# Kernel tuning notes

Hardware: AMD Instinct MI355X
Metric: run time of the kernel (lower is better)

The kernel has to match this reference:

```python
import jax, jax.numpy as jnp
import numpy as np

N0, N1, N2, N3, N4 = 50000, 150000, 20000, 5000, 1000
E0, E1, NNZ01 = 800000, 1500000, 300000
D, CCI = 64, 3


def _xavier(key, shape):
    fan_in, fan_out = shape[0], shape[-1]
    s = jnp.sqrt(2.0 / (fan_in + fan_out)).astype(jnp.float32)
    return jax.random.normal(key, shape, dtype=jnp.float32) * s


def setup_inputs() -> dict:
    ks = jax.random.split(jax.random.key(0), 24)
    return {
        "x_0": jax.random.normal(ks[0], (N0, D), jnp.float32),
        "x_1": jax.random.normal(ks[1], (N1, D), jnp.float32),
        "x_2": jax.random.normal(ks[2], (N2, D), jnp.float32),
        "x_3": jax.random.normal(ks[3], (N3, D), jnp.float32),
        "x_4": jax.random.normal(ks[4], (N4, D), jnp.float32),
        "adjacency_0_idx": jax.random.randint(ks[5], (2, E0), 0, N0),
        "adjacency_0_val": jax.random.uniform(ks[6], (E0,), jnp.float32),
        "adjacency_1_idx": jax.random.randint(ks[7], (2, E1), 0, N1),
        "adjacency_1_val": jax.random.uniform(ks[8], (E1,), jnp.float32),
        "incidence_0_1_idx": jnp.stack([
            jax.random.randint(ks[9], (NNZ01,), 0, N0),   # row: 0-cells
            jax.random.randint(ks[10], (NNZ01,), 0, N1),  # col: 1-cells
        ]),
        "incidence_0_1_val": jax.random.uniform(ks[11], (NNZ01,), jnp.float32),
        "cci_0_to_0": jax.random.normal(ks[12], (E0, CCI), jnp.float32),
        "cci_1_to_1": jax.random.normal(ks[13], (E1, CCI), jnp.float32),
        "W_hbs0": _xavier(ks[14], (D, D)),
        "a_hbs0": _xavier(ks[15], (CCI,)),
        "W_hbs1": _xavier(ks[16], (D, D)),
        "a_hbs1": _xavier(ks[17], (CCI,)),
        "W_hbns_s": _xavier(ks[18], (D, D)),
        "W_hbns_t": _xavier(ks[19], (D, D)),
        "W_aggr0": _xavier(ks[20], (D, D)),
        "W_aggr1": _xavier(ks[21], (D, D)),
    }


def _hbs(x, idx, val, cci, W, a):
    # same-rank message passing: m = xW, per-nonzero coeff = A_val * (cci . a)
    m = x @ W                                    # (N, D)
    coeff = val * (cci @ a)                      # (E,)
    msg = coeff[:, None] * m[idx[0]]             # gather source rows (E, D)
    return jax.nn.relu(jax.ops.segment_sum(msg, idx[1], num_segments=x.shape[0]))


def reference(x_0, x_1, x_2, x_3, x_4,
              adjacency_0_idx, adjacency_0_val,
              adjacency_1_idx, adjacency_1_val,
              incidence_0_1_idx, incidence_0_1_val,
              cci_0_to_0, cci_1_to_1,
              W_hbs0, a_hbs0, W_hbs1, a_hbs1,
              W_hbns_s, W_hbns_t, W_aggr0, W_aggr1):
    # HBS blocks (rank 0 -> 0 and 1 -> 1)
    x_0_to_0 = _hbs(x_0, adjacency_0_idx, adjacency_0_val, cci_0_to_0, W_hbs0, a_hbs0)
    x_1_to_1 = _hbs(x_1, adjacency_1_idx, adjacency_1_val, cci_1_to_1, W_hbs1, a_hbs1)

    # HBNS block across incidence_0_1 (rows index 0-cells, cols index 1-cells)
    row, col = incidence_0_1_idx[0], incidence_0_1_idx[1]
    ms = x_1 @ W_hbns_s                          # source (1-cell) messages
    mt = x_0 @ W_hbns_t                          # target (0-cell) messages
    v = incidence_0_1_val[:, None]
    x_1_to_0 = jax.nn.relu(jax.ops.segment_sum(v * ms[col], row, num_segments=x_0.shape[0]))
    x_0_to_1 = jax.nn.relu(jax.ops.segment_sum(v * mt[row], col, num_segments=x_1.shape[0]))

    # RankAggregator: sum sources, linear map, update
    x_0_level1 = jax.nn.relu((x_0_to_0 + x_1_to_0) @ W_aggr0)
    x_1_level1 = jax.nn.relu((x_1_to_1 + x_0_to_1) @ W_aggr1)
    return (x_0_level1, x_1_level1, x_2, x_3, x_4)
```

## Files before the change

kernel.cpp:

```cpp
#include <hip/hip_runtime.h>

constexpr int N0 = 50000, N1 = 150000, N2 = 20000, N3 = 5000, N4 = 1000;
constexpr int E0 = 800000, E1 = 1500000, NNZ01 = 300000;
constexpr int D = 64;

__global__ __launch_bounds__(256) void gemm64(const float* __restrict__ x,
                                              const float* __restrict__ W,
                                              float* __restrict__ y, int n) {
    __shared__ float Ws[64][64];
    __shared__ float Xs[64][64];
    const int t = threadIdx.x;
    for (int i = t; i < 64 * 64; i += 256) Ws[i >> 6][i & 63] = W[i];
    const long row0 = (long)blockIdx.x * 64;
    const int nrow = min(64, n - (int)row0);
    {
        const float4* xv = (const float4*)(x + row0 * D);
        float4* xs = (float4*)&Xs[0][0];
        for (int i = t; i < nrow * 16; i += 256) xs[i] = xv[i];
    }
    __syncthreads();
    const int r0 = (t >> 4) * 4;
    const int c  = (t & 15) * 4;
    float acc[4][4] = {};
#pragma unroll
    for (int k = 0; k < 64; ++k) {
        const float4 w = *(const float4*)&Ws[k][c];
#pragma unroll
        for (int rr = 0; rr < 4; ++rr) {
            const float xv = Xs[r0 + rr][k];
            acc[rr][0] = fmaf(xv, w.x, acc[rr][0]);
            acc[rr][1] = fmaf(xv, w.y, acc[rr][1]);
            acc[rr][2] = fmaf(xv, w.z, acc[rr][2]);
            acc[rr][3] = fmaf(xv, w.w, acc[rr][3]);
        }
    }
#pragma unroll
    for (int rr = 0; rr < 4; ++rr) {
        const long row = row0 + r0 + rr;
        if (row < n) {
            *(float4*)(y + row * D + c) =
                make_float4(acc[rr][0], acc[rr][1], acc[rr][2], acc[rr][3]);
        }
    }
}

__global__ __launch_bounds__(256) void gemm64_aggr(const float* __restrict__ A,
                                                   const float* __restrict__ B,
                                                   const float* __restrict__ W,
                                                   float* __restrict__ y, int n) {
    __shared__ float Ws[64][64];
    __shared__ float Xs[64][64];
    const int t = threadIdx.x;
    for (int i = t; i < 64 * 64; i += 256) Ws[i >> 6][i & 63] = W[i];
    const long row0 = (long)blockIdx.x * 64;
    const int nrow = min(64, n - (int)row0);
    {
        const float4* av = (const float4*)(A + row0 * D);
        const float4* bv = (const float4*)(B + row0 * D);
        float4* xs = (float4*)&Xs[0][0];
        for (int i = t; i < nrow * 16; i += 256) {
            const float4 p = av[i];
            const float4 q = bv[i];
            float4 r;
            r.x = fmaxf(p.x, 0.f) + fmaxf(q.x, 0.f);
            r.y = fmaxf(p.y, 0.f) + fmaxf(q.y, 0.f);
            r.z = fmaxf(p.z, 0.f) + fmaxf(q.z, 0.f);
            r.w = fmaxf(p.w, 0.f) + fmaxf(q.w, 0.f);
            xs[i] = r;
        }
    }
    __syncthreads();
    const int r0 = (t >> 4) * 4;
    const int c  = (t & 15) * 4;
    float acc[4][4] = {};
#pragma unroll
    for (int k = 0; k < 64; ++k) {
        const float4 w = *(const float4*)&Ws[k][c];
#pragma unroll
        for (int rr = 0; rr < 4; ++rr) {
            const float xv = Xs[r0 + rr][k];
            acc[rr][0] = fmaf(xv, w.x, acc[rr][0]);
            acc[rr][1] = fmaf(xv, w.y, acc[rr][1]);
            acc[rr][2] = fmaf(xv, w.z, acc[rr][2]);
            acc[rr][3] = fmaf(xv, w.w, acc[rr][3]);
        }
    }
#pragma unroll
    for (int rr = 0; rr < 4; ++rr) {
        const long row = row0 + r0 + rr;
        if (row < n) {
            float4 o;
            o.x = fmaxf(acc[rr][0], 0.f);
            o.y = fmaxf(acc[rr][1], 0.f);
            o.z = fmaxf(acc[rr][2], 0.f);
            o.w = fmaxf(acc[rr][3], 0.f);
            *(float4*)(y + row * D + c) = o;
        }
    }
}

__global__ __launch_bounds__(256) void hbs_scatter(const int* __restrict__ src,
                                                   const int* __restrict__ dst,
                                                   const float* __restrict__ val,
                                                   const float* __restrict__ cci,
                                                   const float* __restrict__ a,
                                                   const float* __restrict__ m,
                                                   float* __restrict__ acc, int ne) {
    const int e = blockIdx.x * 4 + (threadIdx.x >> 6);
    if (e >= ne) return;
    const int lane = threadIdx.x & 63;
    const int s = src[e];
    const int d = dst[e];
    const float coeff =
        val[e] * (cci[(size_t)e * 3 + 0] * a[0] + cci[(size_t)e * 3 + 1] * a[1] +
                  cci[(size_t)e * 3 + 2] * a[2]);
    atomicAdd(&acc[(size_t)d * D + lane], coeff * m[(size_t)s * D + lane]);
}

__global__ __launch_bounds__(256) void hbns_scatter(const int* __restrict__ rowi,
                                                    const int* __restrict__ coli,
                                                    const float* __restrict__ val,
                                                    const float* __restrict__ ms,
                                                    const float* __restrict__ mt,
                                                    float* __restrict__ acc10,
                                                    float* __restrict__ acc01, int ne) {
    const int e = blockIdx.x * 4 + (threadIdx.x >> 6);
    if (e >= ne) return;
    const int lane = threadIdx.x & 63;
    const int r = rowi[e];
    const int c = coli[e];
    const float v = val[e];
    atomicAdd(&acc10[(size_t)r * D + lane], v * ms[(size_t)c * D + lane]);
    atomicAdd(&acc01[(size_t)c * D + lane], v * mt[(size_t)r * D + lane]);
}

extern "C" void kernel_launch(void* const* d_in, const int* in_sizes, int n_in,
                              void* d_out, int out_size, void* d_ws, size_t ws_size,
                              hipStream_t stream) {
    const float* x0    = (const float*)d_in[0];
    const float* x1    = (const float*)d_in[1];
    const float* x2    = (const float*)d_in[2];
    const float* x3    = (const float*)d_in[3];
    const float* x4    = (const float*)d_in[4];
    const int*   adj0  = (const int*)d_in[5];
    const float* adj0v = (const float*)d_in[6];
    const int*   adj1  = (const int*)d_in[7];
    const float* adj1v = (const float*)d_in[8];
    const int*   inc01 = (const int*)d_in[9];
    const float* incv  = (const float*)d_in[10];
    const float* cci0  = (const float*)d_in[11];
    const float* cci1  = (const float*)d_in[12];
    const float* Whbs0 = (const float*)d_in[13];
    const float* ahbs0 = (const float*)d_in[14];
    const float* Whbs1 = (const float*)d_in[15];
    const float* ahbs1 = (const float*)d_in[16];
    const float* Wns_s = (const float*)d_in[17];
    const float* Wns_t = (const float*)d_in[18];
    const float* Wagg0 = (const float*)d_in[19];
    const float* Wagg1 = (const float*)d_in[20];

    float* out = (float*)d_out;
    float* ws  = (float*)d_ws;

    const size_t S0 = (size_t)N0 * D;
    const size_t S1 = (size_t)N1 * D;

    const size_t full_bytes = (2 * S0 + 2 * S1) * 2 * sizeof(float);
    float *m0, *m1, *msb, *mtb, *acc00, *acc11, *acc10, *acc01;
    if (ws_size >= full_bytes) {
        m0 = ws;            m1 = m0 + S0;
        msb = m1 + S1;      mtb = msb + S1;
        acc00 = mtb + S0;   acc11 = acc00 + S0;
        acc10 = acc11 + S1; acc01 = acc10 + S0;
    } else {
        m0 = out;           m1 = out + S0;
        msb = ws;           mtb = msb + S1;
        acc00 = mtb + S0;   acc11 = acc00 + S0;
        acc10 = acc11 + S1; acc01 = acc10 + S0;
    }

    hipMemsetAsync(acc00, 0, (2 * S0 + 2 * S1) * sizeof(float), stream);

    gemm64<<<(N0 + 63) / 64, 256, 0, stream>>>(x0, Whbs0, m0, N0);
    gemm64<<<(N1 + 63) / 64, 256, 0, stream>>>(x1, Whbs1, m1, N1);
    gemm64<<<(N1 + 63) / 64, 256, 0, stream>>>(x1, Wns_s, msb, N1);
    gemm64<<<(N0 + 63) / 64, 256, 0, stream>>>(x0, Wns_t, mtb, N0);

    hbs_scatter<<<(E0 + 3) / 4, 256, 0, stream>>>(adj0, adj0 + E0, adj0v, cci0,
                                                  ahbs0, m0, acc00, E0);
    hbs_scatter<<<(E1 + 3) / 4, 256, 0, stream>>>(adj1, adj1 + E1, adj1v, cci1,
                                                  ahbs1, m1, acc11, E1);
    hbns_scatter<<<(NNZ01 + 3) / 4, 256, 0, stream>>>(inc01, inc01 + NNZ01, incv,
                                                      msb, mtb, acc10, acc01, NNZ01);

    gemm64_aggr<<<(N0 + 63) / 64, 256, 0, stream>>>(acc00, acc10, Wagg0, out, N0);
    gemm64_aggr<<<(N1 + 63) / 64, 256, 0, stream>>>(acc11, acc01, Wagg1, out + S0, N1);

    hipMemcpyAsync(out + S0 + S1, x2, (size_t)N2 * D * sizeof(float),
                   hipMemcpyDeviceToDevice, stream);
    hipMemcpyAsync(out + S0 + S1 + (size_t)N2 * D, x3, (size_t)N3 * D * sizeof(float),
                   hipMemcpyDeviceToDevice, stream);
    hipMemcpyAsync(out + S0 + S1 + (size_t)(N2 + N3) * D, x4,
                   (size_t)N4 * D * sizeof(float), hipMemcpyDeviceToDevice, stream);
}
```

Baseline: 1.140 ms.

## Replace atomic edge scatter with CSR counting-sort and per-node segmented gather

Builds per-destination CSR offsets on each call: an integer histogram, a three-pass prefix scan, then an atomic-cursor reorder of edge ids. The float per-lane atomic scatter is replaced by a per-node wavefront gather that accumulates in registers and fuses the ReLU. The aggregation GEMM then reads the pre-summed buffer written into the output in place, which drops the zeroing memset of large accumulators. The cost is several extra launches plus integer atomics for the sort, and the workspace-size fallback path is removed.

```diff
diff --git a/kernel.cpp b/kernel.cpp
--- a/kernel.cpp
+++ b/kernel.cpp
@@ -4,6 +4,12 @@
 constexpr int E0 = 800000, E1 = 1500000, NNZ01 = 300000;
 constexpr int D = 64;
 
+constexpr int TOT_NODES = 2 * N0 + 2 * N1;
+constexpr int OFFN = TOT_NODES + 1;
+constexpr int SCAN_CHUNK = 2048;
+constexpr int NB = (OFFN + SCAN_CHUNK - 1) / SCAN_CHUNK;
+
+template <bool RELU_STORE>
 __global__ __launch_bounds__(256) void gemm64(const float* __restrict__ x,
                                               const float* __restrict__ W,
                                               float* __restrict__ y, int n) {
@@ -38,100 +44,147 @@
     for (int rr = 0; rr < 4; ++rr) {
         const long row = row0 + r0 + rr;
         if (row < n) {
-            *(float4*)(y + row * D + c) =
-                make_float4(acc[rr][0], acc[rr][1], acc[rr][2], acc[rr][3]);
-        }
-    }
-}
-
-__global__ __launch_bounds__(256) void gemm64_aggr(const float* __restrict__ A,
-                                                   const float* __restrict__ B,
-                                                   const float* __restrict__ W,
-                                                   float* __restrict__ y, int n) {
-    __shared__ float Ws[64][64];
-    __shared__ float Xs[64][64];
+            float4 o = make_float4(acc[rr][0], acc[rr][1], acc[rr][2], acc[rr][3]);
+            if (RELU_STORE) {
+                o.x = fmaxf(o.x, 0.f); o.y = fmaxf(o.y, 0.f);
+                o.z = fmaxf(o.z, 0.f); o.w = fmaxf(o.w, 0.f);
+            }
+            *(float4*)(y + row * D + c) = o;
+        }
+    }
+}
+
+__global__ __launch_bounds__(256) void hbs_prep(const int* __restrict__ dst,
+                                                const float* __restrict__ val,
+                                                const float* __restrict__ cci,
+                                                const float* __restrict__ a,
+                                                float* __restrict__ coeff,
+                                                int* __restrict__ cnt, int ne) {
+    const float a0 = a[0], a1 = a[1], a2 = a[2];
+    for (int e = blockIdx.x * 256 + threadIdx.x; e < ne; e += gridDim.x * 256) {
+        const size_t b = (size_t)e * 3;
+        coeff[e] = val[e] * (cci[b] * a0 + cci[b + 1] * a1 + cci[b + 2] * a2);
+        atomicAdd(&cnt[dst[e]], 1);
+    }
+}
+
+__global__ __launch_bounds__(256) void hist2(const int* __restrict__ row,
+                                             const int* __restrict__ col,
+                                             int* __restrict__ cntA,
+                                             int* __restrict__ cntB, int ne) {
+    for (int e = blockIdx.x * 256 + threadIdx.x; e < ne; e += gridDim.x * 256) {
+        atomicAdd(&cntA[row[e]], 1);
+        atomicAdd(&cntB[col[e]], 1);
+    }
+}
+
+__global__ __launch_bounds__(256) void scan1(int* __restrict__ data,
+                                             int* __restrict__ bsum, int n) {
+    __shared__ int lds[256];
     const int t = threadIdx.x;
-    for (int i = t; i < 64 * 64; i += 256) Ws[i >> 6][i & 63] = W[i];
-    const long row0 = (long)blockIdx.x * 64;
-    const int nrow = min(64, n - (int)row0);
-    {
-        const float4* av = (const float4*)(A + row0 * D);
-        const float4* bv = (const float4*)(B + row0 * D);
-        float4* xs = (float4*)&Xs[0][0];
-        for (int i = t; i < nrow * 16; i += 256) {
-            const float4 p = av[i];
-            const float4 q = bv[i];
-            float4 r;
-            r.x = fmaxf(p.x, 0.f) + fmaxf(q.x, 0.f);
-            r.y = fmaxf(p.y, 0.f) + fmaxf(q.y, 0.f);
-            r.z = fmaxf(p.z, 0.f) + fmaxf(q.z, 0.f);
-            r.w = fmaxf(p.w, 0.f) + fmaxf(q.w, 0.f);
-            xs[i] = r;
-        }
-    }
+    const int base = blockIdx.x * SCAN_CHUNK + t * 8;
+    int v[8]; int tot = 0;
+#pragma unroll
+    for (int j = 0; j < 8; ++j) {
+        const int i = base + j;
+        const int x = (i < n) ? data[i] : 0;
+        v[j] = tot; tot += x;
+    }
+    lds[t] = tot;
     __syncthreads();
-    const int r0 = (t >> 4) * 4;
-    const int c  = (t & 15) * 4;
-    float acc[4][4] = {};
-#pragma unroll
-    for (int k = 0; k < 64; ++k) {
-        const float4 w = *(const float4*)&Ws[k][c];
-#pragma unroll
-        for (int rr = 0; rr < 4; ++rr) {
-            const float xv = Xs[r0 + rr][k];
-            acc[rr][0] = fmaf(xv, w.x, acc[rr][0]);
-            acc[rr][1] = fmaf(xv, w.y, acc[rr][1]);
-            acc[rr][2] = fmaf(xv, w.z, acc[rr][2]);
-            acc[rr][3] = fmaf(xv, w.w, acc[rr][3]);
-        }
-    }
-#pragma unroll
-    for (int rr = 0; rr < 4; ++rr) {
-        const long row = row0 + r0 + rr;
-        if (row < n) {
-            float4 o;
-            o.x = fmaxf(acc[rr][0], 0.f);
-            o.y = fmaxf(acc[rr][1], 0.f);
-            o.z = fmaxf(acc[rr][2], 0.f);
-            o.w = fmaxf(acc[rr][3], 0.f);
-            *(float4*)(y + row * D + c) = o;
-        }
-    }
-}
-
-__global__ __launch_bounds__(256) void hbs_scatter(const int* __restrict__ src,
-                                                   const int* __restrict__ dst,
-                                                   const float* __restrict__ val,
-                                                   const float* __restrict__ cci,
-                                                   const float* __restrict__ a,
-                                                   const float* __restrict__ m,
-                                                   float* __restrict__ acc, int ne) {
-    const int e = blockIdx.x * 4 + (threadIdx.x >> 6);
-    if (e >= ne) return;
+    for (int off = 1; off < 256; off <<= 1) {
+        const int y = (t >= off) ? lds[t - off] : 0;
+        __syncthreads();
+        lds[t] += y;
+        __syncthreads();
+    }
+    const int excl = lds[t] - tot;
+    if (t == 255) bsum[blockIdx.x] = lds[255];
+#pragma unroll
+    for (int j = 0; j < 8; ++j) {
+        const int i = base + j;
+        if (i < n) data[i] = excl + v[j];
+    }
+}
+
+__global__ __launch_bounds__(256) void scan2(int* __restrict__ bsum, int nb) {
+    __shared__ int lds[256];
+    const int t = threadIdx.x;
+    const int x = (t < nb) ? bsum[t] : 0;
+    lds[t] = x;
+    __syncthreads();
+    for (int off = 1; off < 256; off <<= 1) {
+        const int y = (t >= off) ? lds[t - off] : 0;
+        __syncthreads();
+        lds[t] += y;
+        __syncthreads();
+    }
+    if (t < nb) bsum[t] = lds[t] - x;
+}
+
+__global__ __launch_bounds__(256) void scan3(int* __restrict__ data,
+                                             const int* __restrict__ bsum, int n) {
+    const int add = bsum[blockIdx.x];
+    const int base = blockIdx.x * SCAN_CHUNK + threadIdx.x * 8;
+#pragma unroll
+    for (int j = 0; j < 8; ++j) {
+        const int i = base + j;
+        if (i < n) data[i] += add;
+    }
+}
+
+__global__ __launch_bounds__(256) void reorder1(const int* __restrict__ dst,
+                                                int* __restrict__ cursor,
+                                                int* __restrict__ order, int ne) {
+    for (int e = blockIdx.x * 256 + threadIdx.x; e < ne; e += gridDim.x * 256) {
+        const int pos = atomicAdd(&cursor[dst[e]], 1);
+        order[pos] = e;
+    }
+}
+
+__global__ __launch_bounds__(256) void reorder2(const int* __restrict__ row,
+                                                const int* __restrict__ col,
+                                                int* __restrict__ curA,
+                                                int* __restrict__ curB,
+                                                int* __restrict__ order, int ne) {
+    for (int e = blockIdx.x * 256 + threadIdx.x; e < ne; e += gridDim.x * 256) {
+        const int pA = atomicAdd(&curA[row[e]], 1);
+        order[pA] = e;
+        const int pB = atomicAdd(&curB[col[e]], 1);
+        order[pB] = e;
+    }
+}
+
+template <bool ADD>
+__global__ __launch_bounds__(256) void seg_accum(const int* __restrict__ order,
+                                                 const int* __restrict__ offsets,
+                                                 const int* __restrict__ src,
+                                                 const float* __restrict__ coeff,
+                                                 const float* __restrict__ m,
+                                                 float* __restrict__ outbuf, int n) {
+    const int node = blockIdx.x * 4 + (threadIdx.x >> 6);
+    if (node >= n) return;
     const int lane = threadIdx.x & 63;
-    const int s = src[e];
-    const int d = dst[e];
-    const float coeff =
-        val[e] * (cci[(size_t)e * 3 + 0] * a[0] + cci[(size_t)e * 3 + 1] * a[1] +
-                  cci[(size_t)e * 3 + 2] * a[2]);
-    atomicAdd(&acc[(size_t)d * D + lane], coeff * m[(size_t)s * D + lane]);
-}
-
-__global__ __launch_bounds__(256) void hbns_scatter(const int* __restrict__ rowi,
-                                                    const int* __restrict__ coli,
-                                                    const float* __restrict__ val,
-                                                    const float* __restrict__ ms,
-                                                    const float* __restrict__ mt,
-                                                    float* __restrict__ acc10,
-                                                    float* __restrict__ acc01, int ne) {
-    const int e = blockIdx.x * 4 + (threadIdx.x >> 6);
-    if (e >= ne) return;
-    const int lane = threadIdx.x & 63;
-    const int r = rowi[e];
-    const int c = coli[e];
-    const float v = val[e];
-    atomicAdd(&acc10[(size_t)r * D + lane], v * ms[(size_t)c * D + lane]);
-    atomicAdd(&acc01[(size_t)c * D + lane], v * mt[(size_t)r * D + lane]);
+    const int beg = offsets[node];
+    const int end = offsets[node + 1];
+    float acc = 0.f;
+    for (int base = beg; base < end; base += 64) {
+        const int nn = min(64, end - base);
+        int s_l = 0; float c_l = 0.f;
+        if (lane < nn) {
+            const int eid = order[base + lane];
+            s_l = src[eid];
+            c_l = coeff[eid];
+        }
+        for (int j = 0; j < nn; ++j) {
+            const int s = __shfl(s_l, j);
+            const float c = __shfl(c_l, j);
+            acc = fmaf(c, m[(size_t)s * D + lane], acc);
+        }
+    }
+    const float r = fmaxf(acc, 0.f);
+    float* o = outbuf + (size_t)node * D + lane;
+    if (ADD) *o += r; else *o = r;
 }
 
 extern "C" void kernel_launch(void* const* d_in, const int* in_sizes, int n_in,
@@ -160,41 +213,61 @@
     const float* Wagg1 = (const float*)d_in[20];
 
     float* out = (float*)d_out;
-    float* ws  = (float*)d_ws;
 
     const size_t S0 = (size_t)N0 * D;
     const size_t S1 = (size_t)N1 * D;
 
-    const size_t full_bytes = (2 * S0 + 2 * S1) * 2 * sizeof(float);
-    float *m0, *m1, *msb, *mtb, *acc00, *acc11, *acc10, *acc01;
-    if (ws_size >= full_bytes) {
-        m0 = ws;            m1 = m0 + S0;
-        msb = m1 + S1;      mtb = msb + S1;
-        acc00 = mtb + S0;   acc11 = acc00 + S0;
-        acc10 = acc11 + S1; acc01 = acc10 + S0;
-    } else {
-        m0 = out;           m1 = out + S0;
-        msb = ws;           mtb = msb + S1;
-        acc00 = mtb + S0;   acc11 = acc00 + S0;
-        acc10 = acc11 + S1; acc01 = acc10 + S0;
-    }
-
-    hipMemsetAsync(acc00, 0, (2 * S0 + 2 * S1) * sizeof(float), stream);
-
-    gemm64<<<(N0 + 63) / 64, 256, 0, stream>>>(x0, Whbs0, m0, N0);
-    gemm64<<<(N1 + 63) / 64, 256, 0, stream>>>(x1, Whbs1, m1, N1);
-    gemm64<<<(N1 + 63) / 64, 256, 0, stream>>>(x1, Wns_s, msb, N1);
-    gemm64<<<(N0 + 63) / 64, 256, 0, stream>>>(x0, Wns_t, mtb, N0);
-
-    hbs_scatter<<<(E0 + 3) / 4, 256, 0, stream>>>(adj0, adj0 + E0, adj0v, cci0,
-                                                  ahbs0, m0, acc00, E0);
-    hbs_scatter<<<(E1 + 3) / 4, 256, 0, stream>>>(adj1, adj1 + E1, adj1v, cci1,
-                                                  ahbs1, m1, acc11, E1);
-    hbns_scatter<<<(NNZ01 + 3) / 4, 256, 0, stream>>>(inc01, inc01 + NNZ01, incv,
-                                                      msb, mtb, acc10, acc01, NNZ01);
-
-    gemm64_aggr<<<(N0 + 63) / 64, 256, 0, stream>>>(acc00, acc10, Wagg0, out, N0);
-    gemm64_aggr<<<(N1 + 63) / 64, 256, 0, stream>>>(acc11, acc01, Wagg1, out + S0, N1);
+    float* m0     = (float*)d_ws;
+    float* m1     = m0 + S0;
+    float* msb    = m1 + S1;
+    float* mtb    = msb + S1;
+    float* coeff0 = mtb + S0;
+    float* coeff1 = coeff0 + E0;
+    int*   offs   = (int*)(coeff1 + E1);
+    int*   bsum   = offs + OFFN;
+    int*   cursor = bsum + 256;
+    int*   order  = cursor + TOT_NODES;
+
+    float* s00 = out;
+    float* s11 = out + S0;
+
+    hipMemsetAsync(offs, 0, OFFN * sizeof(int), stream);
+
+    gemm64<false><<<(N0 + 63) / 64, 256, 0, stream>>>(x0, Whbs0, m0, N0);
+    gemm64<false><<<(N1 + 63) / 64, 256, 0, stream>>>(x1, Whbs1, m1, N1);
+    gemm64<false><<<(N1 + 63) / 64, 256, 0, stream>>>(x1, Wns_s, msb, N1);
+    gemm64<false><<<(N0 + 63) / 64, 256, 0, stream>>>(x0, Wns_t, mtb, N0);
+
+    hbs_prep<<<1024, 256, 0, stream>>>(adj0 + E0, adj0v, cci0, ahbs0, coeff0,
+                                       offs, E0);
+    hbs_prep<<<2048, 256, 0, stream>>>(adj1 + E1, adj1v, cci1, ahbs1, coeff1,
+                                       offs + N0, E1);
+    hist2<<<1024, 256, 0, stream>>>(inc01, inc01 + NNZ01, offs + N0 + N1,
+                                    offs + 2 * N0 + N1, NNZ01);
+
+    scan1<<<NB, 256, 0, stream>>>(offs, bsum, OFFN);
+    scan2<<<1, 256, 0, stream>>>(bsum, NB);
+    scan3<<<NB, 256, 0, stream>>>(offs, bsum, OFFN);
+
+    hipMemcpyAsync(cursor, offs, TOT_NODES * sizeof(int),
+                   hipMemcpyDeviceToDevice, stream);
+    reorder1<<<1024, 256, 0, stream>>>(adj0 + E0, cursor, order, E0);
+    reorder1<<<2048, 256, 0, stream>>>(adj1 + E1, cursor + N0, order, E1);
+    reorder2<<<1024, 256, 0, stream>>>(inc01, inc01 + NNZ01, cursor + N0 + N1,
+                                       cursor + 2 * N0 + N1, order, NNZ01);
+
+    seg_accum<false><<<(N0 + 3) / 4, 256, 0, stream>>>(order, offs, adj0, coeff0,
+                                                       m0, s00, N0);
+    seg_accum<false><<<(N1 + 3) / 4, 256, 0, stream>>>(order, offs + N0, adj1,
+                                                       coeff1, m1, s11, N1);
+    seg_accum<true><<<(N0 + 3) / 4, 256, 0, stream>>>(order, offs + N0 + N1,
+                                                      inc01 + NNZ01, incv, msb,
+                                                      s00, N0);
+    seg_accum<true><<<(N1 + 3) / 4, 256, 0, stream>>>(order, offs + 2 * N0 + N1,
+                                                      inc01, incv, mtb, s11, N1);
+
+    gemm64<true><<<(N0 + 63) / 64, 256, 0, stream>>>(s00, Wagg0, out, N0);
+    gemm64<true><<<(N1 + 63) / 64, 256, 0, stream>>>(s11, Wagg1, out + S0, N1);
 
     hipMemcpyAsync(out + S0 + S1, x2, (size_t)N2 * D * sizeof(float),
                    hipMemcpyDeviceToDevice, stream);
```

After: 1.106 ms. 2.9% less time.

## Bucket edges by destination and accumulate in shared memory instead of global atomics

Applied to the files above, without the earlier changes.

Replaces per-edge global float atomics with a counting sort of edges into 128-row destination buckets (histogram, scan, expand into packed records). Each bucket is then accumulated in shared memory by one block, and the ReLU and source-sum are applied at write-out. It also fuses the pairs of input GEMMs that share an input into one dual-weight kernel, and runs the aggregation GEMM in place on the output buffer. The aim is to remove global atomic contention and the large accumulator memset. The cost is extra preprocessing passes with atomic cursors, a serial single-block scan, and a workspace-size assumption that is no longer checked.

```diff
diff --git a/kernel.cpp b/kernel.cpp
--- a/kernel.cpp
+++ b/kernel.cpp
@@ -4,6 +4,70 @@
 constexpr int E0 = 800000, E1 = 1500000, NNZ01 = 300000;
 constexpr int D = 64;
 
+constexpr int BROWS = 128;
+constexpr int NBKT00 = (N0 + BROWS - 1) / BROWS;
+constexpr int NBKT11 = (N1 + BROWS - 1) / BROWS;
+constexpr int BKT_BASE00 = 0;
+constexpr int BKT_BASE11 = NBKT00;
+constexpr int BKT_BASE10 = NBKT00 + NBKT11;
+constexpr int BKT_BASE01 = 2 * NBKT00 + NBKT11;
+constexpr int NBKT_TOT = 2 * NBKT00 + 2 * NBKT11;
+constexpr int NREC = E0 + E1 + 2 * NNZ01;
+
+__global__ __launch_bounds__(256) void gemm64_dual(const float* __restrict__ x,
+                                                   const float* __restrict__ Wa,
+                                                   const float* __restrict__ Wb,
+                                                   float* __restrict__ ya,
+                                                   float* __restrict__ yb, int n) {
+    __shared__ float Ws[2][64][64];
+    __shared__ float Xs[64][64];
+    const int t = threadIdx.x;
+    for (int i = t; i < 64 * 64; i += 256) {
+        Ws[0][i >> 6][i & 63] = Wa[i];
+        Ws[1][i >> 6][i & 63] = Wb[i];
+    }
+    const long row0 = (long)blockIdx.x * 64;
+    const int nrow = min(64, n - (int)row0);
+    {
+        const float4* xv = (const float4*)(x + row0 * D);
+        float4* xs = (float4*)&Xs[0][0];
+        for (int i = t; i < nrow * 16; i += 256) xs[i] = xv[i];
+    }
+    __syncthreads();
+    const int r0 = (t >> 4) * 4;
+    const int c  = (t & 15) * 4;
+    float acca[4][4] = {};
+    float accb[4][4] = {};
+#pragma unroll
+    for (int k = 0; k < 64; ++k) {
+        const float4 wa = *(const float4*)&Ws[0][k][c];
+        const float4 wb = *(const float4*)&Ws[1][k][c];
+#pragma unroll
+        for (int rr = 0; rr < 4; ++rr) {
+            const float xv = Xs[r0 + rr][k];
+            acca[rr][0] = fmaf(xv, wa.x, acca[rr][0]);
+            acca[rr][1] = fmaf(xv, wa.y, acca[rr][1]);
+            acca[rr][2] = fmaf(xv, wa.z, acca[rr][2]);
+            acca[rr][3] = fmaf(xv, wa.w, acca[rr][3]);
+            accb[rr][0] = fmaf(xv, wb.x, accb[rr][0]);
+            accb[rr][1] = fmaf(xv, wb.y, accb[rr][1]);
+            accb[rr][2] = fmaf(xv, wb.z, accb[rr][2]);
+            accb[rr][3] = fmaf(xv, wb.w, accb[rr][3]);
+        }
+    }
+#pragma unroll
+    for (int rr = 0; rr < 4; ++rr) {
+        const long row = row0 + r0 + rr;
+        if (row < n) {
+            *(float4*)(ya + row * D + c) =
+                make_float4(acca[rr][0], acca[rr][1], acca[rr][2], acca[rr][3]);
+            *(float4*)(yb + row * D + c) =
+                make_float4(accb[rr][0], accb[rr][1], accb[rr][2], accb[rr][3]);
+        }
+    }
+}
+
+template <bool RELU_STORE>
 __global__ __launch_bounds__(256) void gemm64(const float* __restrict__ x,
                                               const float* __restrict__ W,
                                               float* __restrict__ y, int n) {
@@ -38,100 +102,134 @@
     for (int rr = 0; rr < 4; ++rr) {
         const long row = row0 + r0 + rr;
         if (row < n) {
-            *(float4*)(y + row * D + c) =
-                make_float4(acc[rr][0], acc[rr][1], acc[rr][2], acc[rr][3]);
-        }
-    }
-}
-
-__global__ __launch_bounds__(256) void gemm64_aggr(const float* __restrict__ A,
-                                                   const float* __restrict__ B,
-                                                   const float* __restrict__ W,
-                                                   float* __restrict__ y, int n) {
-    __shared__ float Ws[64][64];
-    __shared__ float Xs[64][64];
+            float4 o = make_float4(acc[rr][0], acc[rr][1], acc[rr][2], acc[rr][3]);
+            if (RELU_STORE) {
+                o.x = fmaxf(o.x, 0.f); o.y = fmaxf(o.y, 0.f);
+                o.z = fmaxf(o.z, 0.f); o.w = fmaxf(o.w, 0.f);
+            }
+            *(float4*)(y + row * D + c) = o;
+        }
+    }
+}
+
+__global__ __launch_bounds__(256) void count_hist(const int* __restrict__ dst,
+                                                  int ne, int nbkt,
+                                                  int* __restrict__ gcount) {
+    __shared__ int hist[NBKT11];
+    for (int i = threadIdx.x; i < nbkt; i += 256) hist[i] = 0;
+    __syncthreads();
+    for (int e = blockIdx.x * 256 + threadIdx.x; e < ne; e += gridDim.x * 256)
+        atomicAdd(&hist[dst[e] >> 7], 1);
+    __syncthreads();
+    for (int i = threadIdx.x; i < nbkt; i += 256) {
+        const int h = hist[i];
+        if (h) atomicAdd(&gcount[i], h);
+    }
+}
+
+__global__ __launch_bounds__(256) void scan_small(int* __restrict__ data, int n) {
+    __shared__ int lds[256];
+    __shared__ int carry_s;
     const int t = threadIdx.x;
-    for (int i = t; i < 64 * 64; i += 256) Ws[i >> 6][i & 63] = W[i];
-    const long row0 = (long)blockIdx.x * 64;
-    const int nrow = min(64, n - (int)row0);
-    {
-        const float4* av = (const float4*)(A + row0 * D);
-        const float4* bv = (const float4*)(B + row0 * D);
-        float4* xs = (float4*)&Xs[0][0];
-        for (int i = t; i < nrow * 16; i += 256) {
-            const float4 p = av[i];
-            const float4 q = bv[i];
-            float4 r;
-            r.x = fmaxf(p.x, 0.f) + fmaxf(q.x, 0.f);
-            r.y = fmaxf(p.y, 0.f) + fmaxf(q.y, 0.f);
-            r.z = fmaxf(p.z, 0.f) + fmaxf(q.z, 0.f);
-            r.w = fmaxf(p.w, 0.f) + fmaxf(q.w, 0.f);
-            xs[i] = r;
-        }
-    }
-    __syncthreads();
-    const int r0 = (t >> 4) * 4;
-    const int c  = (t & 15) * 4;
-    float acc[4][4] = {};
-#pragma unroll
-    for (int k = 0; k < 64; ++k) {
-        const float4 w = *(const float4*)&Ws[k][c];
-#pragma unroll
-        for (int rr = 0; rr < 4; ++rr) {
-            const float xv = Xs[r0 + rr][k];
-            acc[rr][0] = fmaf(xv, w.x, acc[rr][0]);
-            acc[rr][1] = fmaf(xv, w.y, acc[rr][1]);
-            acc[rr][2] = fmaf(xv, w.z, acc[rr][2]);
-            acc[rr][3] = fmaf(xv, w.w, acc[rr][3]);
-        }
-    }
-#pragma unroll
-    for (int rr = 0; rr < 4; ++rr) {
-        const long row = row0 + r0 + rr;
-        if (row < n) {
-            float4 o;
-            o.x = fmaxf(acc[rr][0], 0.f);
-            o.y = fmaxf(acc[rr][1], 0.f);
-            o.z = fmaxf(acc[rr][2], 0.f);
-            o.w = fmaxf(acc[rr][3], 0.f);
-            *(float4*)(y + row * D + c) = o;
-        }
-    }
-}
-
-__global__ __launch_bounds__(256) void hbs_scatter(const int* __restrict__ src,
-                                                   const int* __restrict__ dst,
-                                                   const float* __restrict__ val,
-                                                   const float* __restrict__ cci,
-                                                   const float* __restrict__ a,
-                                                   const float* __restrict__ m,
-                                                   float* __restrict__ acc, int ne) {
-    const int e = blockIdx.x * 4 + (threadIdx.x >> 6);
-    if (e >= ne) return;
-    const int lane = threadIdx.x & 63;
-    const int s = src[e];
-    const int d = dst[e];
-    const float coeff =
-        val[e] * (cci[(size_t)e * 3 + 0] * a[0] + cci[(size_t)e * 3 + 1] * a[1] +
-                  cci[(size_t)e * 3 + 2] * a[2]);
-    atomicAdd(&acc[(size_t)d * D + lane], coeff * m[(size_t)s * D + lane]);
-}
-
-__global__ __launch_bounds__(256) void hbns_scatter(const int* __restrict__ rowi,
-                                                    const int* __restrict__ coli,
-                                                    const float* __restrict__ val,
-                                                    const float* __restrict__ ms,
-                                                    const float* __restrict__ mt,
-                                                    float* __restrict__ acc10,
-                                                    float* __restrict__ acc01, int ne) {
-    const int e = blockIdx.x * 4 + (threadIdx.x >> 6);
-    if (e >= ne) return;
-    const int lane = threadIdx.x & 63;
-    const int r = rowi[e];
-    const int c = coli[e];
-    const float v = val[e];
-    atomicAdd(&acc10[(size_t)r * D + lane], v * ms[(size_t)c * D + lane]);
-    atomicAdd(&acc01[(size_t)c * D + lane], v * mt[(size_t)r * D + lane]);
+    if (t == 0) carry_s = 0;
+    __syncthreads();
+    for (int base = 0; base < n; base += 256) {
+        const int i = base + t;
+        const int x = (i < n) ? data[i] : 0;
+        lds[t] = x;
+        __syncthreads();
+        for (int off = 1; off < 256; off <<= 1) {
+            const int y = (t >= off) ? lds[t - off] : 0;
+            __syncthreads();
+            lds[t] += y;
+            __syncthreads();
+        }
+        const int incl = lds[t];
+        const int carry = carry_s;
+        __syncthreads();
+        if (i < n) data[i] = carry + incl - x;
+        if (t == 255) carry_s = carry + incl;
+        __syncthreads();
+    }
+}
+
+__global__ __launch_bounds__(256) void expand_hbs(const int* __restrict__ src,
+                                                  const int* __restrict__ dst,
+                                                  const float* __restrict__ val,
+                                                  const float* __restrict__ cci,
+                                                  const float* __restrict__ a,
+                                                  int* __restrict__ cursor,
+                                                  int bktbase,
+                                                  int2* __restrict__ rec, int ne) {
+    const float a0 = a[0], a1 = a[1], a2 = a[2];
+    for (int e = blockIdx.x * 256 + threadIdx.x; e < ne; e += gridDim.x * 256) {
+        const int d = dst[e];
+        const size_t b3 = (size_t)e * 3;
+        const float coeff =
+            val[e] * (cci[b3] * a0 + cci[b3 + 1] * a1 + cci[b3 + 2] * a2);
+        const int pos = atomicAdd(&cursor[bktbase + (d >> 7)], 1);
+        rec[pos] = make_int2(src[e] | ((d & 127) << 20), __float_as_int(coeff));
+    }
+}
+
+__global__ __launch_bounds__(256) void expand_inc(const int* __restrict__ row,
+                                                  const int* __restrict__ col,
+                                                  const float* __restrict__ val,
+                                                  int* __restrict__ cursor,
+                                                  int2* __restrict__ rec, int ne) {
+    for (int e = blockIdx.x * 256 + threadIdx.x; e < ne; e += gridDim.x * 256) {
+        const int r = row[e], c = col[e];
+        const int vb = __float_as_int(val[e]);
+        const int p1 = atomicAdd(&cursor[BKT_BASE10 + (r >> 7)], 1);
+        rec[p1] = make_int2(c | ((r & 127) << 20), vb);
+        const int p2 = atomicAdd(&cursor[BKT_BASE01 + (c >> 7)], 1);
+        rec[p2] = make_int2(r | ((c & 127) << 20), vb);
+    }
+}
+
+template <bool ADD>
+__global__ __launch_bounds__(256) void bucket_accum(const int2* __restrict__ rec,
+                                                    const int* __restrict__ bases,
+                                                    int dirbase,
+                                                    const float* __restrict__ m,
+                                                    float* __restrict__ outbuf,
+                                                    int n) {
+    __shared__ float acc[BROWS * 64];
+    __shared__ int2 stg[4][64];
+    const int t = threadIdx.x;
+    const int lane = t & 63;
+    const int wid = t >> 6;
+    for (int i = t * 4; i < BROWS * 64; i += 1024)
+        *(float4*)&acc[i] = make_float4(0.f, 0.f, 0.f, 0.f);
+    __syncthreads();
+    const int beg = bases[dirbase + blockIdx.x];
+    const int end = bases[dirbase + blockIdx.x + 1];
+    for (int base = beg + wid * 64; base < end; base += 256) {
+        const int nn = min(64, end - base);
+        if (lane < nn) stg[wid][lane] = rec[base + lane];
+        for (int j = 0; j < nn; ++j) {
+            const int2 r = stg[wid][j];
+            const float c = __int_as_float(r.y);
+            const int s = r.x & 0xFFFFF;
+            const int dl = r.x >> 20;
+            atomicAdd(&acc[dl * 64 + lane], c * m[(size_t)s * D + lane]);
+        }
+    }
+    __syncthreads();
+    const long r0 = (long)blockIdx.x * BROWS;
+    const int nrow = min(BROWS, n - (int)r0);
+    float* o = outbuf + r0 * D;
+    for (int i = t * 4; i < nrow * 64; i += 1024) {
+        const float4 v = *(const float4*)&acc[i];
+        float4 w;
+        w.x = fmaxf(v.x, 0.f); w.y = fmaxf(v.y, 0.f);
+        w.z = fmaxf(v.z, 0.f); w.w = fmaxf(v.w, 0.f);
+        if (ADD) {
+            const float4 e = *(const float4*)&o[i];
+            w.x += e.x; w.y += e.y; w.z += e.z; w.w += e.w;
+        }
+        *(float4*)&o[i] = w;
+    }
 }
 
 extern "C" void kernel_launch(void* const* d_in, const int* in_sizes, int n_in,
@@ -160,41 +258,53 @@
     const float* Wagg1 = (const float*)d_in[20];
 
     float* out = (float*)d_out;
-    float* ws  = (float*)d_ws;
 
     const size_t S0 = (size_t)N0 * D;
     const size_t S1 = (size_t)N1 * D;
 
-    const size_t full_bytes = (2 * S0 + 2 * S1) * 2 * sizeof(float);
-    float *m0, *m1, *msb, *mtb, *acc00, *acc11, *acc10, *acc01;
-    if (ws_size >= full_bytes) {
-        m0 = ws;            m1 = m0 + S0;
-        msb = m1 + S1;      mtb = msb + S1;
-        acc00 = mtb + S0;   acc11 = acc00 + S0;
-        acc10 = acc11 + S1; acc01 = acc10 + S0;
-    } else {
-        m0 = out;           m1 = out + S0;
-        msb = ws;           mtb = msb + S1;
-        acc00 = mtb + S0;   acc11 = acc00 + S0;
-        acc10 = acc11 + S1; acc01 = acc10 + S0;
-    }
-
-    hipMemsetAsync(acc00, 0, (2 * S0 + 2 * S1) * sizeof(float), stream);
-
-    gemm64<<<(N0 + 63) / 64, 256, 0, stream>>>(x0, Whbs0, m0, N0);
-    gemm64<<<(N1 + 63) / 64, 256, 0, stream>>>(x1, Whbs1, m1, N1);
-    gemm64<<<(N1 + 63) / 64, 256, 0, stream>>>(x1, Wns_s, msb, N1);
-    gemm64<<<(N0 + 63) / 64, 256, 0, stream>>>(x0, Wns_t, mtb, N0);
-
-    hbs_scatter<<<(E0 + 3) / 4, 256, 0, stream>>>(adj0, adj0 + E0, adj0v, cci0,
-                                                  ahbs0, m0, acc00, E0);
-    hbs_scatter<<<(E1 + 3) / 4, 256, 0, stream>>>(adj1, adj1 + E1, adj1v, cci1,
-                                                  ahbs1, m1, acc11, E1);
-    hbns_scatter<<<(NNZ01 + 3) / 4, 256, 0, stream>>>(inc01, inc01 + NNZ01, incv,
-                                                      msb, mtb, acc10, acc01, NNZ01);
-
-    gemm64_aggr<<<(N0 + 63) / 64, 256, 0, stream>>>(acc00, acc10, Wagg0, out, N0);
-    gemm64_aggr<<<(N1 + 63) / 64, 256, 0, stream>>>(acc11, acc01, Wagg1, out + S0, N1);
+    float* m0   = (float*)d_ws;
+    float* m1   = m0 + S0;
+    float* msb  = m1 + S1;
+    float* mtb  = msb + S1;
+    int2*  rec  = (int2*)(mtb + S0);
+    int*   bases  = (int*)(rec + NREC);
+    int*   cursor = bases + NBKT_TOT + 1;
+
+    float* s00 = out;
+    float* s11 = out + S0;
+
+    hipMemsetAsync(bases, 0, (NBKT_TOT + 1) * sizeof(int), stream);
+
+    gemm64_dual<<<(N0 + 63) / 64, 256, 0, stream>>>(x0, Whbs0, Wns_t, m0, mtb, N0);
+    gemm64_dual<<<(N1 + 63) / 64, 256, 0, stream>>>(x1, Whbs1, Wns_s, m1, msb, N1);
+
+    count_hist<<<128, 256, 0, stream>>>(adj0 + E0, E0, NBKT00, bases + BKT_BASE00);
+    count_hist<<<192, 256, 0, stream>>>(adj1 + E1, E1, NBKT11, bases + BKT_BASE11);
+    count_hist<<<64, 256, 0, stream>>>(inc01, NNZ01, NBKT00, bases + BKT_BASE10);
+    count_hist<<<64, 256, 0, stream>>>(inc01 + NNZ01, NNZ01, NBKT11, bases + BKT_BASE01);
+
+    scan_small<<<1, 256, 0, stream>>>(bases, NBKT_TOT + 1);
+    hipMemcpyAsync(cursor, bases, NBKT_TOT * sizeof(int),
+                   hipMemcpyDeviceToDevice, stream);
+
+    expand_hbs<<<512, 256, 0, stream>>>(adj0, adj0 + E0, adj0v, cci0, ahbs0,
+                                        cursor, BKT_BASE00, rec, E0);
+    expand_hbs<<<1024, 256, 0, stream>>>(adj1, adj1 + E1, adj1v, cci1, ahbs1,
+                                         cursor, BKT_BASE11, rec, E1);
+    expand_inc<<<256, 256, 0, stream>>>(inc01, inc01 + NNZ01, incv, cursor, rec,
+                                        NNZ01);
+
+    bucket_accum<false><<<NBKT00, 256, 0, stream>>>(rec, bases, BKT_BASE00, m0,
+                                                    s00, N0);
+    bucket_accum<false><<<NBKT11, 256, 0, stream>>>(rec, bases, BKT_BASE11, m1,
+                                                    s11, N1);
+    bucket_accum<true><<<NBKT00, 256, 0, stream>>>(rec, bases, BKT_BASE10, msb,
+                                                   s00, N0);
+    bucket_accum<true><<<NBKT11, 256, 0, stream>>>(rec, bases, BKT_BASE01, mtb,
+                                                   s11, N1);
+
+    gemm64<true><<<(N0 + 63) / 64, 256, 0, stream>>>(s00, Wagg0, out, N0);
+    gemm64<true><<<(N1 + 63) / 64, 256, 0, stream>>>(s11, Wagg1, out + S0, N1);
 
     hipMemcpyAsync(out + S0 + S1, x2, (size_t)N2 * D * sizeof(float),
                    hipMemcpyDeviceToDevice, stream);
```

Result: slower. 3.261 ms (+186.2%).
